# Kernel optimization log

Hardware: AMD Instinct MI355X
Metric: run time of the kernel (lower is better)

Reference implementation:

```python
import jax, jax.numpy as jnp
import numpy as np

F8_MAX = 448.0  # float8_e4m3fn max
F4_MAX = 6.0    # fp4 e2m1 max
BLOCK = 16      # NVFP4 scaling block size along K

# representable |values| of fp4 e2m1 and midpoints for nearest rounding
_LEVELS = jnp.array([0.0, 0.5, 1.0, 1.5, 2.0, 3.0, 4.0, 6.0], dtype=jnp.float32)
_MIDS = (_LEVELS[:-1] + _LEVELS[1:]) * 0.5


def _e2m1_round(a):
    # round-to-nearest fp4 e2m1 value, sign-magnitude
    s = jnp.sign(a)
    m = jnp.clip(jnp.abs(a), 0.0, F4_MAX)
    idx = jnp.searchsorted(_MIDS, m, side='left')
    return s * jnp.take(_LEVELS, idx)


def _e4m3(x):
    # quantize to float8 e4m3 and dequantize back to fp32
    return jnp.clip(x, -F8_MAX, F8_MAX).astype(jnp.float8_e4m3fn).astype(jnp.float32)


def nvfp4_fake_quant(x, s2):
    # x: [..., K]; s2: scalar global scale = 448*6/global_amax
    shp = x.shape
    K = shp[-1]
    xb = x.reshape(shp[:-1] + (K // BLOCK, BLOCK))  # [..., K/16, 16]
    amax = jnp.max(jnp.abs(xb), axis=-1, keepdims=True)
    sf = _e4m3(amax * s2 / F4_MAX)          # stored per-block fp8 scale (cutlass_vec)
    scale = sf / s2                          # per-block dequant scale in real units
    safe = jnp.where(scale > 0.0, scale, 1.0)
    q = _e2m1_round(xb / safe)               # fp4 codes (as values)
    deq = jnp.where(scale > 0.0, q * scale, 0.0)
    return deq.reshape(shp)


def setup_inputs() -> dict:
    key = jax.random.key(0)
    kx, kw, kb, ks = jax.random.split(key, 4)
    K, N = 4096, 4096
    x = jax.random.normal(kx, (4, 2048, K), dtype=jnp.float32)
    weight = jax.random.uniform(kw, (N, K), dtype=jnp.float32)
    bias = jax.random.uniform(kb, (N,), dtype=jnp.float32)
    # fp4_global_scale of a rand(1, K) tensor, as done in the module __init__
    dummy = jax.random.uniform(ks, (1, K), dtype=jnp.float32)
    s_in2 = ((F8_MAX * F4_MAX) / jnp.max(jnp.abs(dummy))).reshape(1)
    return {'x': x, 'weight': weight, 'bias': bias, 's_in2': s_in2}


def reference(x, weight, bias, s_in2):
    s2_in = s_in2.reshape(())
    s2_w = (F8_MAX * F4_MAX) / jnp.max(jnp.abs(weight))  # fp4_global_scale(weight)
    x_dq = nvfp4_fake_quant(x, s2_in)        # fake-quant activations
    w_dq = nvfp4_fake_quant(weight, s2_w)    # dequantized fp4 weight (stored at init)
    # F.linear: [b,s,k] @ [n,k]^T + bias
    return jnp.einsum('bsk,nk->bsn', x_dq, w_dq) + bias
```

## Files before the change

kernel.cpp:

```cpp
#include <hip/hip_runtime.h>
#include <hip/hip_bf16.h>

typedef __attribute__((ext_vector_type(8))) short short8;
typedef __attribute__((ext_vector_type(8))) unsigned short ushort8;
typedef __attribute__((ext_vector_type(4))) float f32x4;
typedef unsigned short ushort;

#define K_DIM 4096
#define N_DIM 4096
#define BK 32
#define NT (K_DIM / BK)


__device__ __forceinline__ float e4m3_rne(float v) {
    if (v >= 0.015625f) {
        unsigned u = __float_as_uint(v);
        unsigned lsb = (u >> 20) & 1u;
        u = (u + 0x7FFFFu + lsb) & 0xFFF00000u;
        return __uint_as_float(u);
    }
    return rintf(v * 512.0f) * 0.001953125f;
}

__device__ __forceinline__ float e2m1_level(float m) {
    float lv = 0.0f;
    lv = (m > 0.25f) ? 0.5f : lv;
    lv = (m > 0.75f) ? 1.0f : lv;
    lv = (m > 1.25f) ? 1.5f : lv;
    lv = (m > 1.75f) ? 2.0f : lv;
    lv = (m > 2.5f)  ? 3.0f : lv;
    lv = (m > 3.5f)  ? 4.0f : lv;
    lv = (m > 5.0f)  ? 6.0f : lv;
    return lv;
}

__device__ __forceinline__ ushort f32_to_bf16_bits(float f) {
    unsigned u = __float_as_uint(f);
    return (ushort)((u + 0x7FFFu + ((u >> 16) & 1u)) >> 16);
}


__global__ void wamax_kernel(const float* __restrict__ w, unsigned* amax_bits, int n4) {
    float m = 0.f;
    const f32x4* w4 = (const f32x4*)w;
    for (int i = blockIdx.x * blockDim.x + threadIdx.x; i < n4; i += gridDim.x * blockDim.x) {
        f32x4 v = w4[i];
        m = fmaxf(m, fmaxf(fmaxf(fabsf(v.x), fabsf(v.y)), fmaxf(fabsf(v.z), fabsf(v.w))));
    }
#pragma unroll
    for (int off = 32; off >= 1; off >>= 1)
        m = fmaxf(m, __shfl_down(m, off));
    __shared__ float red[4];
    const int lane = threadIdx.x & 63, wv = threadIdx.x >> 6;
    if (lane == 0) red[wv] = m;
    __syncthreads();
    if (threadIdx.x == 0) {
        m = fmaxf(fmaxf(red[0], red[1]), fmaxf(red[2], red[3]));
        atomicMax(amax_bits, __float_as_uint(m));
    }
}

__global__ void quant_both_kernel(const float* __restrict__ x,
                                  const float* __restrict__ w,
                                  const float* __restrict__ s2_ptr,
                                  const unsigned* __restrict__ amax_bits,
                                  ushort* __restrict__ xq,
                                  ushort* __restrict__ wq, int nx, int ntot) {
    int t = blockIdx.x * blockDim.x + threadIdx.x;
    if (t >= ntot) return;
    const float* src;
    ushort* dst;
    float s2;
    if (t < nx) {
        src = x; dst = xq; s2 = *s2_ptr;
    } else {
        src = w; dst = wq; t -= nx;
        s2 = 2688.0f / __uint_as_float(*amax_bits);
    }

    const f32x4* s = (const f32x4*)src + (size_t)t * 4;
    float vals[16];
    f32x4 v0 = s[0], v1 = s[1], v2 = s[2], v3 = s[3];
#pragma unroll
    for (int i = 0; i < 4; ++i) {
        vals[i] = v0[i]; vals[4 + i] = v1[i]; vals[8 + i] = v2[i]; vals[12 + i] = v3[i];
    }
    float amax = 0.f;
#pragma unroll
    for (int i = 0; i < 16; ++i) amax = fmaxf(amax, fabsf(vals[i]));

    float sf = e4m3_rne(fminf(amax * s2 / 6.0f, 448.0f));
    float scale = sf / s2;

    ushort8 o0, o1;
    if (scale > 0.f) {
#pragma unroll
        for (int i = 0; i < 16; ++i) {
            float r = vals[i] / scale;
            float m = fminf(fabsf(r), 6.0f);
            float q = copysignf(e2m1_level(m), r);
            ushort b = f32_to_bf16_bits(q * scale);
            if (i < 8) o0[i] = b; else o1[i - 8] = b;
        }
    } else {
#pragma unroll
        for (int i = 0; i < 8; ++i) { o0[i] = 0; o1[i] = 0; }
    }
    ushort8* d8 = (ushort8*)(dst + (size_t)t * 16);
    d8[0] = o0;
    d8[1] = o1;
}


__device__ __forceinline__ void gload16(const ushort* g, ushort* l) {
    __builtin_amdgcn_global_load_lds(
        (const __attribute__((address_space(1))) void*)g,
        (__attribute__((address_space(3))) void*)l, 16, 0, 0);
}

#define VM4 asm volatile("s_waitcnt vmcnt(4)" ::: "memory")
#define VM0 asm volatile("s_waitcnt vmcnt(0)" ::: "memory")
#define BAR asm volatile("s_barrier" ::: "memory")

__global__ __launch_bounds__(512, 2) void gemm8(
    const ushort* __restrict__ Aq, const ushort* __restrict__ Bq,
    const float* __restrict__ bias, float* __restrict__ C) {
    __shared__ ushort lds[4 * 16384];

    const int tid  = threadIdx.x;
    const int lane = tid & 63;
    const int wave = tid >> 6;
    const int wr = wave >> 2;
    const int wc = wave & 3;

    const int swz = blockIdx.x;
    const int grp = swz >> 8, lcl = swz & 255;
    const int by = grp * 16 + (lcl & 15);
    const int bx = lcl >> 4;
    const int bm = by * 256, bn = bx * 256;

    const int r0  = tid >> 2;
    const int cg0 = ((tid & 3) - ((r0 >> 1) & 3)) & 3;
    const ushort* sA0 = Aq + (size_t)(bm + r0) * K_DIM + cg0 * 8;
    const ushort* sB0 = Bq + (size_t)(bn + r0) * K_DIM + cg0 * 8;
    ushort* dA0 = &lds[wave * 512];
    ushort* dB0 = &lds[8192 + wave * 512];

    const int pr   = ((lane >> 4) + ((lane & 15) >> 1)) & 3;
    const int idxA = (wr * 128 + (lane & 15)) * 32 + pr * 8;
    const int idxB = 8192 + (wc * 64 + (lane & 15)) * 32 + pr * 8;

    f32x4 acc[8][4];
#pragma unroll
    for (int m = 0; m < 8; ++m)
#pragma unroll
        for (int n = 0; n < 4; ++n) acc[m][n] = (f32x4)(0.f);

    short8 af[8], bfr[4];

#define SA(t) { const size_t ko = (size_t)(t) * BK; const int bb = ((t) & 3) * 16384; \
    gload16(sA0 + ko, dA0 + bb); gload16(sA0 + (size_t)128 * K_DIM + ko, dA0 + bb + 4096); }
#define SB(t) { const size_t ko = (size_t)(t) * BK; const int bb = ((t) & 3) * 16384; \
    gload16(sB0 + ko, dB0 + bb); gload16(sB0 + (size_t)128 * K_DIM + ko, dB0 + bb + 4096); }

#define READ_ALO(bb) _Pragma("unroll") for (int m = 0; m < 4; ++m) \
        af[m] = *(const short8*)&lds[(bb) + idxA + m * 512];
#define READ_AHI(bb) _Pragma("unroll") for (int m = 0; m < 4; ++m) \
        af[4 + m] = *(const short8*)&lds[(bb) + idxA + (4 + m) * 512];
#define READ_B(bb)   _Pragma("unroll") for (int n = 0; n < 4; ++n) \
        bfr[n] = *(const short8*)&lds[(bb) + idxB + n * 512];

#define MML                                                                   \
    __builtin_amdgcn_s_setprio(1);                                            \
    _Pragma("unroll") for (int m = 0; m < 4; ++m)                             \
    _Pragma("unroll") for (int n = 0; n < 4; ++n)                             \
        acc[m][n] = __builtin_amdgcn_mfma_f32_16x16x32_bf16(af[m], bfr[n], acc[m][n], 0, 0, 0); \
    __builtin_amdgcn_s_setprio(0);
#define MMH                                                                   \
    __builtin_amdgcn_s_setprio(1);                                            \
    _Pragma("unroll") for (int m = 4; m < 8; ++m)                             \
    _Pragma("unroll") for (int n = 0; n < 4; ++n)                             \
        acc[m][n] = __builtin_amdgcn_mfma_f32_16x16x32_bf16(af[m], bfr[n], acc[m][n], 0, 0, 0); \
    __builtin_amdgcn_s_setprio(0);

    SA(0); SB(0); SA(1); SB(1); SA(2); SB(2);
    VM4; BAR;
    READ_ALO(0); READ_B(0);

#pragma unroll 1
    for (int t = 0; t <= NT - 4; ++t) {
        const int bb  = (t & 3) * 16384;
        const int bb1 = ((t + 1) & 3) * 16384;
        VM4; BAR;
        READ_AHI(bb);
        SA(t + 3);
        MML;
        READ_ALO(bb1);
        SB(t + 3);
        MMH;
        READ_B(bb1);
    }
    {
        const int bb  = ((NT - 3) & 3) * 16384;
        const int bb1 = ((NT - 2) & 3) * 16384;
        VM4; BAR;
        READ_AHI(bb);
        MML;
        READ_ALO(bb1);
        MMH;
        READ_B(bb1);
    }
    {
        const int bb  = ((NT - 2) & 3) * 16384;
        const int bb1 = ((NT - 1) & 3) * 16384;
        VM0; BAR;
        READ_AHI(bb);
        MML;
        READ_ALO(bb1);
        MMH;
        READ_B(bb1);
    }
    {
        const int bb = ((NT - 1) & 3) * 16384;
        READ_AHI(bb);
        MML;
        MMH;
    }

    const int fq = lane >> 4, fr = lane & 15;
    float bv[4];
#pragma unroll
    for (int n = 0; n < 4; ++n) bv[n] = bias[bn + wc * 64 + n * 16 + fr];
#pragma unroll
    for (int m = 0; m < 8; ++m)
#pragma unroll
        for (int r = 0; r < 4; ++r) {
            const int row = bm + wr * 128 + m * 16 + fq * 4 + r;
            float* Cr = C + (size_t)row * N_DIM + bn + wc * 64 + fr;
#pragma unroll
            for (int n = 0; n < 4; ++n) Cr[n * 16] = acc[m][n][r] + bv[n];
        }
#undef SA
#undef SB
#undef READ_ALO
#undef READ_AHI
#undef READ_B
#undef MML
#undef MMH
}


extern "C" void kernel_launch(void* const* d_in, const int* in_sizes, int n_in,
                              void* d_out, int out_size, void* d_ws, size_t ws_size,
                              hipStream_t stream) {
    const float* x     = (const float*)d_in[0];
    const float* w     = (const float*)d_in[1];
    const float* bias  = (const float*)d_in[2];
    const float* s_in2 = (const float*)d_in[3];
    float* out = (float*)d_out;

    const int M = in_sizes[0] / K_DIM;

    unsigned* amax_bits = (unsigned*)d_ws;
    ushort* xq = (ushort*)((char*)d_ws + 256);
    ushort* wq = (ushort*)((char*)d_ws + 256 + (size_t)M * K_DIM * 2);

    hipMemsetAsync(amax_bits, 0, 4, stream);
    wamax_kernel<<<1024, 256, 0, stream>>>(w, amax_bits, (N_DIM * K_DIM) / 4);

    const int nx = (M * K_DIM) / 16;
    const int nw = (N_DIM * K_DIM) / 16;
    quant_both_kernel<<<(nx + nw) / 256, 256, 0, stream>>>(
        x, w, s_in2, amax_bits, xq, wq, nx, nx + nw);

    const int nwg = (M / 256) * (N_DIM / 256);
    gemm8<<<nwg, 512, 0, stream>>>(xq, wq, bias, out);
}
```

Before: 291.1 us.

## Switch GEMM inner loop to 32x32x16 bf16 MFMA tiles

```diff
diff --git a/kernel.cpp b/kernel.cpp
--- a/kernel.cpp
+++ b/kernel.cpp
@@ -4,6 +4,7 @@
 typedef __attribute__((ext_vector_type(8))) short short8;
 typedef __attribute__((ext_vector_type(8))) unsigned short ushort8;
 typedef __attribute__((ext_vector_type(4))) float f32x4;
+typedef __attribute__((ext_vector_type(16))) float f32x16;
 typedef unsigned short ushort;
 
 #define K_DIM 4096
@@ -146,107 +147,111 @@
     ushort* dA0 = &lds[wave * 512];
     ushort* dB0 = &lds[8192 + wave * 512];
 
-    const int pr   = ((lane >> 4) + ((lane & 15) >> 1)) & 3;
-    const int idxA = (wr * 128 + (lane & 15)) * 32 + pr * 8;
-    const int idxB = 8192 + (wc * 64 + (lane & 15)) * 32 + pr * 8;
-
-    f32x4 acc[8][4];
-#pragma unroll
-    for (int m = 0; m < 8; ++m)
-#pragma unroll
-        for (int n = 0; n < 4; ++n) acc[m][n] = (f32x4)(0.f);
-
-    short8 af[8], bfr[4];
+    const int rowA = wr * 128 + (lane & 31);
+    const int rowB = wc * 64 + (lane & 31);
+    const int kg   = lane >> 5;
+    const int idxA0 = rowA * 32 + (((kg)     + (rowA >> 1)) & 3) * 8;
+    const int idxA1 = rowA * 32 + (((kg + 2) + (rowA >> 1)) & 3) * 8;
+    const int idxB0 = 8192 + rowB * 32 + (((kg)     + (rowB >> 1)) & 3) * 8;
+    const int idxB1 = 8192 + rowB * 32 + (((kg + 2) + (rowB >> 1)) & 3) * 8;
+
+    f32x16 acc[4][2];
+#pragma unroll
+    for (int m = 0; m < 4; ++m)
+#pragma unroll
+        for (int n = 0; n < 2; ++n) acc[m][n] = (f32x16)(0.f);
+
+    short8 a0[4], a1[4], b0[2], b1[2];
 
 #define SA(t) { const size_t ko = (size_t)(t) * BK; const int bb = ((t) & 3) * 16384; \
     gload16(sA0 + ko, dA0 + bb); gload16(sA0 + (size_t)128 * K_DIM + ko, dA0 + bb + 4096); }
 #define SB(t) { const size_t ko = (size_t)(t) * BK; const int bb = ((t) & 3) * 16384; \
     gload16(sB0 + ko, dB0 + bb); gload16(sB0 + (size_t)128 * K_DIM + ko, dB0 + bb + 4096); }
 
-#define READ_ALO(bb) _Pragma("unroll") for (int m = 0; m < 4; ++m) \
-        af[m] = *(const short8*)&lds[(bb) + idxA + m * 512];
-#define READ_AHI(bb) _Pragma("unroll") for (int m = 0; m < 4; ++m) \
-        af[4 + m] = *(const short8*)&lds[(bb) + idxA + (4 + m) * 512];
-#define READ_B(bb)   _Pragma("unroll") for (int n = 0; n < 4; ++n) \
-        bfr[n] = *(const short8*)&lds[(bb) + idxB + n * 512];
-
-#define MML                                                                   \
+#define READ_K0(bb) {                                                         \
+    _Pragma("unroll") for (int m = 0; m < 4; ++m)                             \
+        a0[m] = *(const short8*)&lds[(bb) + idxA0 + m * 1024];                \
+    _Pragma("unroll") for (int n = 0; n < 2; ++n)                             \
+        b0[n] = *(const short8*)&lds[(bb) + idxB0 + n * 1024]; }
+#define READ_K1(bb) {                                                         \
+    _Pragma("unroll") for (int m = 0; m < 4; ++m)                             \
+        a1[m] = *(const short8*)&lds[(bb) + idxA1 + m * 1024];                \
+    _Pragma("unroll") for (int n = 0; n < 2; ++n)                             \
+        b1[n] = *(const short8*)&lds[(bb) + idxB1 + n * 1024]; }
+
+#define MM0                                                                   \
     __builtin_amdgcn_s_setprio(1);                                            \
     _Pragma("unroll") for (int m = 0; m < 4; ++m)                             \
-    _Pragma("unroll") for (int n = 0; n < 4; ++n)                             \
-        acc[m][n] = __builtin_amdgcn_mfma_f32_16x16x32_bf16(af[m], bfr[n], acc[m][n], 0, 0, 0); \
+    _Pragma("unroll") for (int n = 0; n < 2; ++n)                             \
+        acc[m][n] = __builtin_amdgcn_mfma_f32_32x32x16_bf16(a0[m], b0[n], acc[m][n], 0, 0, 0); \
     __builtin_amdgcn_s_setprio(0);
-#define MMH                                                                   \
+#define MM1                                                                   \
     __builtin_amdgcn_s_setprio(1);                                            \
-    _Pragma("unroll") for (int m = 4; m < 8; ++m)                             \
-    _Pragma("unroll") for (int n = 0; n < 4; ++n)                             \
-        acc[m][n] = __builtin_amdgcn_mfma_f32_16x16x32_bf16(af[m], bfr[n], acc[m][n], 0, 0, 0); \
+    _Pragma("unroll") for (int m = 0; m < 4; ++m)                             \
+    _Pragma("unroll") for (int n = 0; n < 2; ++n)                             \
+        acc[m][n] = __builtin_amdgcn_mfma_f32_32x32x16_bf16(a1[m], b1[n], acc[m][n], 0, 0, 0); \
     __builtin_amdgcn_s_setprio(0);
 
     SA(0); SB(0); SA(1); SB(1); SA(2); SB(2);
     VM4; BAR;
-    READ_ALO(0); READ_B(0);
+    READ_K0(0);
 
 #pragma unroll 1
     for (int t = 0; t <= NT - 4; ++t) {
         const int bb  = (t & 3) * 16384;
         const int bb1 = ((t + 1) & 3) * 16384;
         VM4; BAR;
-        READ_AHI(bb);
+        READ_K1(bb);
         SA(t + 3);
-        MML;
-        READ_ALO(bb1);
+        MM0;
+        READ_K0(bb1);
         SB(t + 3);
-        MMH;
-        READ_B(bb1);
+        MM1;
     }
     {
         const int bb  = ((NT - 3) & 3) * 16384;
         const int bb1 = ((NT - 2) & 3) * 16384;
         VM4; BAR;
-        READ_AHI(bb);
-        MML;
-        READ_ALO(bb1);
-        MMH;
-        READ_B(bb1);
+        READ_K1(bb);
+        MM0;
+        READ_K0(bb1);
+        MM1;
     }
     {
         const int bb  = ((NT - 2) & 3) * 16384;
         const int bb1 = ((NT - 1) & 3) * 16384;
         VM0; BAR;
-        READ_AHI(bb);
-        MML;
-        READ_ALO(bb1);
-        MMH;
-        READ_B(bb1);
+        READ_K1(bb);
+        MM0;
+        READ_K0(bb1);
+        MM1;
     }
     {
         const int bb = ((NT - 1) & 3) * 16384;
-        READ_AHI(bb);
-        MML;
-        MMH;
-    }
-
-    const int fq = lane >> 4, fr = lane & 15;
-    float bv[4];
-#pragma unroll
-    for (int n = 0; n < 4; ++n) bv[n] = bias[bn + wc * 64 + n * 16 + fr];
-#pragma unroll
-    for (int m = 0; m < 8; ++m)
-#pragma unroll
-        for (int r = 0; r < 4; ++r) {
-            const int row = bm + wr * 128 + m * 16 + fq * 4 + r;
-            float* Cr = C + (size_t)row * N_DIM + bn + wc * 64 + fr;
-#pragma unroll
-            for (int n = 0; n < 4; ++n) Cr[n * 16] = acc[m][n][r] + bv[n];
+        READ_K1(bb);
+        MM0;
+        MM1;
+    }
+
+    const int colb = bn + wc * 64 + (lane & 31);
+    const float bv0 = bias[colb];
+    const float bv1 = bias[colb + 32];
+    const int rbase = bm + wr * 128 + 4 * (lane >> 5);
+#pragma unroll
+    for (int m = 0; m < 4; ++m)
+#pragma unroll
+        for (int reg = 0; reg < 16; ++reg) {
+            const int row = rbase + m * 32 + (reg & 3) + 8 * (reg >> 2);
+            float* Cr = C + (size_t)row * N_DIM + colb;
+            Cr[0]  = acc[m][0][reg] + bv0;
+            Cr[32] = acc[m][1][reg] + bv1;
         }
 #undef SA
 #undef SB
-#undef READ_ALO
-#undef READ_AHI
-#undef READ_B
-#undef MML
-#undef MMH
+#undef READ_K0
+#undef READ_K1
+#undef MM0
+#undef MM1
 }
 
 
```

Result: slower. 322.4 us (+10.8%).
